# Kernel tuning notes

Hardware: AMD Instinct MI355X
Metric: run time of the kernel (lower is better)

The kernel has to match this reference:

```python
import jax, jax.numpy as jnp
import numpy as np

EPS = 1e-3  # matches eps=0.001 in __init__


def p2o(psf, H, W):
    """PSF -> OTF: zero-pad to (H,W), roll so kernel center is at origin, FFT2."""
    B, C, kh, kw = psf.shape
    otf = jnp.zeros((B, C, H, W), psf.dtype).at[:, :, :kh, :kw].set(psf)
    otf = jnp.roll(otf, (-(kh // 2), -(kw // 2)), axis=(-2, -1))
    return jnp.fft.fft2(otf)


def splits_mean(a, sf):
    """Mean over the sf*sf distinct blocks of splits(): contiguous-chunk split
    via view(sf, H/sf, sf, W/sf); mean over the two sf axes equals mean over
    the scale^2 trailing dim of the original splits output."""
    B, C, H, W = a.shape
    return a.reshape(B, C, sf, H // sf, sf, W // sf).mean(axis=(2, 4))


def setup_inputs() -> dict:
    key = jax.random.key(0)
    kx, kk = jax.random.split(key)
    x = jax.random.normal(kx, (4, 64, 128, 128), dtype=jnp.float32)
    k = jax.random.uniform(kk, (4, 64, 25, 25), dtype=jnp.float32)
    alpha = jnp.zeros((1, 64, 1, 1), dtype=jnp.float32)  # learned parameter
    return {"x": x, "k": k, "alpha": alpha, "sf": 2}


def reference(x, k, alpha, sf):
    biaseps = jax.nn.sigmoid(alpha - 9.0) + EPS          # (1,C,1,1)
    B, C, h, w = x.shape
    H, W = h * sf, w * sf
    # s-fold zero-fill upsample (STy)
    STy = jnp.zeros((B, C, H, W), x.dtype).at[:, :, ::sf, ::sf].set(x)
    # nearest-neighbor interpolate by sf
    xu = jnp.repeat(jnp.repeat(x, sf, axis=-2), sf, axis=-1) if sf != 1 else x
    FB = p2o(k, H, W)                                    # complex (B,C,H,W)
    FBC = jnp.conj(FB)
    F2B = jnp.abs(FB) ** 2
    FBFy = FBC * jnp.fft.fft2(STy)
    FR = FBFy + jnp.fft.fft2(biaseps * xu)
    FBR = splits_mean(FB * FR, sf)                       # (B,C,H/sf,W/sf)
    invW = splits_mean(F2B, sf)
    invWBR = FBR / (invW + biaseps)
    FCBinvWBR = FBC * jnp.tile(invWBR, (1, 1, sf, sf))   # repeat(1,1,sf,sf)
    FX = (FR - FCBinvWBR) / biaseps
    return jnp.real(jnp.fft.ifft2(FX))
```

## Files before the change

kernel.cpp:

```cpp
#include <hip/hip_runtime.h>
#include <math.h>


static __device__ __forceinline__ float2 cmul(float2 a, float2 b) {
    return make_float2(a.x * b.x - a.y * b.y, a.x * b.y + a.y * b.x);
}
static __device__ __forceinline__ float2 cadd(float2 a, float2 b) {
    return make_float2(a.x + b.x, a.y + b.y);
}
static __device__ __forceinline__ float2 csub(float2 a, float2 b) {
    return make_float2(a.x - b.x, a.y - b.y);
}
static __device__ __forceinline__ float2 conjf2(float2 a) {
    return make_float2(a.x, -a.y);
}
static __device__ __forceinline__ int PHI(int i) { return i + (i >> 3); }

template <int HB, int SIGN, int THREADS>
static __device__ __forceinline__ void fill_tw(float2* tw) {
    for (int i = threadIdx.x; i < HB; i += THREADS) {
        float s, c;
        __sincosf((float)SIGN * (float)M_PI * (float)i / (float)HB, &s, &c);
        tw[i] = make_float2(c, s);
    }
}

template <int N, int R, int SIGN>
static __device__ __forceinline__ int fft_lds_rows(float2 (&buf)[2][R][N],
                                                   const float2* __restrict__ tw) {
    constexpr int HB = N / 2;
    const int tid = threadIdx.x;
    const int row = tid / HB;
    const int bt = tid % HB;
    int cur = 0, m = 1;
    for (int l = HB; l >= 1; l >>= 1) {
        __syncthreads();
        const int k = bt & (m - 1);
        const float2 w = tw[bt - k];
        float2 a = buf[cur][row][bt];
        float2 b = buf[cur][row][bt + HB];
        float2 d = make_float2(a.x - b.x, a.y - b.y);
        float2 wd = make_float2(w.x * d.x - w.y * d.y, w.x * d.y + w.y * d.x);
        const int o = 2 * bt - k;
        buf[cur ^ 1][row][o] = make_float2(a.x + b.x, a.y + b.y);
        buf[cur ^ 1][row][o + m] = wd;
        cur ^= 1;
        m <<= 1;
    }
    __syncthreads();
    return cur;
}

template <int SIGN, int THREADS>
static __device__ __forceinline__ int fft4_cols_128(float2 (&buf)[2][128][16],
                                                    const float2* __restrict__ tw) {
    const int tid = threadIdx.x;
    int cur = 0, m = 1;
#pragma unroll
    for (int st = 0; st < 3; ++st) {
        __syncthreads();
        for (int w0 = tid; w0 < 512; w0 += THREADS) {
            const int col = w0 & 15;
            const int bq = w0 >> 4;
            const int k = bq & (m - 1);
            const int jm = bq - k;
            const float2 w1 = tw[jm];
            const float2 w2 = tw[2 * jm];
            const float2 w3 = tw[3 * jm];
            float2 a0 = buf[cur][bq][col];
            float2 a1 = buf[cur][bq + 32][col];
            float2 a2 = buf[cur][bq + 64][col];
            float2 a3 = buf[cur][bq + 96][col];
            float2 s02 = cadd(a0, a2), d02 = csub(a0, a2);
            float2 s13 = cadd(a1, a3), d13 = csub(a1, a3);
            float2 b0 = cadd(s02, s13), b2 = csub(s02, s13);
            float2 b1 = make_float2(d02.x - (float)SIGN * d13.y,
                                    d02.y + (float)SIGN * d13.x);
            float2 b3 = make_float2(d02.x + (float)SIGN * d13.y,
                                    d02.y - (float)SIGN * d13.x);
            const int o = 4 * jm + k;
            buf[cur ^ 1][o][col] = b0;
            buf[cur ^ 1][o + m][col] = cmul(w1, b1);
            buf[cur ^ 1][o + 2 * m][col] = cmul(w2, b2);
            buf[cur ^ 1][o + 3 * m][col] = cmul(w3, b3);
        }
        cur ^= 1;
        m <<= 2;
    }
    __syncthreads();
    for (int w0 = tid; w0 < 1024; w0 += THREADS) {
        const int col = w0 & 15;
        const int bt = w0 >> 4;
        float2 a = buf[cur][bt][col];
        float2 b = buf[cur][bt + 64][col];
        buf[cur ^ 1][bt][col] = cadd(a, b);
        buf[cur ^ 1][bt + 64][col] = csub(a, b);
    }
    cur ^= 1;
    __syncthreads();
    return cur;
}

__global__ __launch_bounds__(256) void k1_fft_rows_x(const float* __restrict__ x,
                                                     float2* __restrict__ Fx) {
    __shared__ float2 buf[2][4][128];
    __shared__ float2 tw64m[64];
    const int tid = threadIdx.x;
    const int row = tid >> 6;
    const int t = tid & 63;
    fill_tw<64, -1, 256>(tw64m);
    const int gpair = blockIdx.x * 4 + row;
    const float* r0 = x + (size_t)gpair * 256;
    const float* r1 = r0 + 128;
    const float2 a0 = ((const float2*)r0)[t];
    const float2 a1 = ((const float2*)r1)[t];
    buf[0][row][2 * t].x = a0.x;
    buf[0][row][2 * t].y = a1.x;
    buf[0][row][2 * t + 1].x = a0.y;
    buf[0][row][2 * t + 1].y = a1.y;
    int cur = fft_lds_rows<128, 4, -1>(buf, tw64m);
    float2* d0 = Fx + (size_t)gpair * 256;
    float2* d1 = d0 + 128;
    for (int h = 0; h < 2; ++h) {
        int tt = t + h * 64;
        float2 Zt = buf[cur][row][tt];
        float2 Zm = buf[cur][row][(128 - tt) & 127];
        d0[tt] = make_float2(0.5f * (Zt.x + Zm.x), 0.5f * (Zt.y - Zm.y));
        float ax = Zt.x - Zm.x, ay = Zt.y + Zm.y;
        d1[tt] = make_float2(0.5f * ay, -0.5f * ax);
    }
}

__global__ __launch_bounds__(256) void k2_fft_cols_x(float2* __restrict__ Fx) {
    __shared__ float2 buf[2][128][16];
    __shared__ float2 tw[96];
    const int tid = threadIdx.x;
    const int img = blockIdx.x >> 3;
    const int c0 = (blockIdx.x & 7) * 16;
    for (int i = tid; i < 96; i += 256) {
        float s, c;
        __sincosf(-(float)M_PI * (float)i / 64.f, &s, &c);
        tw[i] = make_float2(c, s);
    }
    float2* base = Fx + (size_t)img * 16384 + c0;
    for (int it = 0; it < 8; ++it) {
        int idx = it * 256 + tid;
        buf[0][idx >> 4][idx & 15] = base[(idx >> 4) * 128 + (idx & 15)];
    }
    int cur = fft4_cols_128<-1, 256>(buf, tw);
    for (int it = 0; it < 8; ++it) {
        int idx = it * 256 + tid;
        base[(idx >> 4) * 128 + (idx & 15)] = buf[cur][idx >> 4][idx & 15];
    }
}

__global__ __launch_bounds__(128) void k3_fft_rows_k(const float* __restrict__ kin,
                                                     float2* __restrict__ FBtmp) {
    __shared__ float2 buf[2][1][256];
    __shared__ float2 tw128m[128];
    const int tid = threadIdx.x;
    const int img = blockIdx.x / 25;
    const int lr = blockIdx.x % 25;
    fill_tw<128, -1, 128>(tw128m);
    const float* krow = kin + img * 625 + lr * 25;
    for (int h = 0; h < 2; ++h) {
        int v = tid + h * 128;
        int pc = (v + 12) & 255;
        buf[0][0][v] = make_float2(pc < 25 ? krow[pc] : 0.f, 0.f);
    }
    int cur = fft_lds_rows<256, 1, -1>(buf, tw128m);
    float2* dst = FBtmp + (size_t)img * 6400 + lr * 256;
    dst[tid] = buf[cur][0][tid];
    dst[tid + 128] = buf[cur][0][tid + 128];
}

__global__ __launch_bounds__(256) void k4_dft_cols_k(const float2* __restrict__ FBtmp,
                                                     float2* __restrict__ FBh) {
    __shared__ float2 T[33][28];
    const int j = threadIdx.x;
    const int img = blockIdx.x >> 2;
    const int q = blockIdx.x & 3;
    const int ubeg = q * 33;
    const int nu = (ubeg + 33 < 129) ? 33 : (129 - ubeg);
    const float k2pi = -2.f * (float)M_PI / 256.f;

    for (int idx = j; idx < nu * 25; idx += 256) {
        const int ul = idx / 25;
        const int p = idx - ul * 25;
        const int u = ubeg + ul;
        float s, c;
        __sincosf(k2pi * (float)((u * (p + 244)) & 255), &s, &c);
        T[ul][p] = make_float2(c, s);
    }

    const float2* src = FBtmp + (size_t)img * 6400 + j;
    float2 S[25];
#pragma unroll
    for (int p = 0; p < 25; ++p) S[p] = src[p * 256];
    __syncthreads();

    float2* dst = FBh + (size_t)img * 33024 + j;
    for (int ul = 0; ul < nu; ++ul) {
        float2 a0 = make_float2(0.f, 0.f);
        float2 a1 = make_float2(0.f, 0.f);
#pragma unroll
        for (int p = 0; p < 25; ++p) {
            const float2 t = T[ul][p];
            const float2 s = S[p];
            if (p & 1) {
                a1.x = fmaf(t.x, s.x, fmaf(-t.y, s.y, a1.x));
                a1.y = fmaf(t.x, s.y, fmaf(t.y, s.x, a1.y));
            } else {
                a0.x = fmaf(t.x, s.x, fmaf(-t.y, s.y, a0.x));
                a0.y = fmaf(t.x, s.y, fmaf(t.y, s.x, a0.y));
            }
        }
        dst[(size_t)(ubeg + ul) * 256] = make_float2(a0.x + a1.x, a0.y + a1.y);
    }
}

__global__ __launch_bounds__(256) void k6_fused(const float2* __restrict__ FBh,
                                                const float2* __restrict__ Fx,
                                                const float* __restrict__ alpha,
                                                float2* __restrict__ Zf) {
    __shared__ float2 stage[4][256];
    __shared__ float2 buf[2][4][288];
    __shared__ float2 tw[192];
    const int tid = threadIdx.x;
    const int rs = tid >> 6;
    const int q = tid & 63;
    const int img = blockIdx.x / 33;
    const int bq = blockIdx.x % 33;
    const int pa = 2 * bq;
    const int pb = (pa + 1 < 65) ? (pa + 1) : 64;
    for (int i = tid; i < 192; i += 256) {
        float s, c;
        __sincosf((float)M_PI * (float)i / 128.f, &s, &c);
        tw[i] = make_float2(c, s);
    }
    {
        const float2* base = FBh + (size_t)img * 33024;
        stage[0][tid] = base[pa * 256 + tid];
        stage[1][tid] = base[(128 - pa) * 256 + tid];
        stage[2][tid] = base[pb * 256 + tid];
        stage[3][tid] = base[(128 - pb) * 256 + tid];
    }
    __syncthreads();

    const int p = (rs < 2) ? pa : pb;
    const int sb = rs & 2;
    const int u = ((rs & 1) == 0) ? p : (128 - p);
    const int um = u & 127;
    const int msel = (um == p) ? 0 : 1;
    const int mi = sb | msel;
    const int oi = sb | (1 - msel);

    const float ci = tw[um].x, si = -tw[um].y;
    const float b = 1.f / (1.f + __expf(9.f - alpha[img & 63])) + 1e-3f;
    const float scale = 1.f / 65536.f;
    const float2 Di0 = make_float2(1.f + ci, si);
    const float2 Di1 = make_float2(1.f - ci, -si);
    const float2 Du = (u < 128) ? Di0 : Di1;
#pragma unroll
    for (int h = 0; h < 2; ++h) {
        const int t = q + 64 * h;
        float2 f00 = stage[mi][t];
        float2 f01 = stage[mi][t + 128];
        float2 f10, f11;
        if (um == 0) {
            f10 = stage[oi][t];
            f11 = stage[oi][t + 128];
        } else {
            f10 = conjf2(stage[oi][(256 - t) & 255]);
            f11 = conjf2(stage[oi][128 - t]);
        }
        float2 fx = Fx[(size_t)img * 16384 + um * 128 + t];
        const float cj = tw[t].x, sj = -tw[t].y;
        float2 Dj0 = make_float2(1.f + cj, sj);
        float2 Dj1 = make_float2(1.f - cj, -sj);
        float2 A = cadd(cmul(f00, Dj0), cmul(f01, Dj1));
        float2 Bt = cadd(cmul(f10, Dj0), cmul(f11, Dj1));
        float2 S1 = cadd(cmul(A, Di0), cmul(Bt, Di1));
        S1.x *= 0.25f;
        S1.y *= 0.25f;
        float S2 = 0.25f * (f00.x * f00.x + f00.y * f00.y + f01.x * f01.x + f01.y * f01.y +
                            f10.x * f10.x + f10.y * f10.y + f11.x * f11.x + f11.y * f11.y);
        float inv = 1.f / (S2 + b);
        float2 mm = make_float2((1.f - S1.x) * inv, (-S1.y) * inv);
        float2 c0v = (u < 128) ? f00 : f10;
        float2 c1v = (u < 128) ? f01 : f11;
        float2 t0 = cadd(cmul(conjf2(c0v), mm), cmul(Du, Dj0));
        float2 t1 = cadd(cmul(conjf2(c1v), mm), cmul(Du, Dj1));
        float2 FX0 = cmul(fx, t0);
        float2 FX1 = cmul(fx, t1);
        buf[0][rs][PHI(t)] = make_float2(FX0.x * scale, FX0.y * scale);
        buf[0][rs][PHI(t + 128)] = make_float2(FX1.x * scale, FX1.y * scale);
    }

    int cur = 0, m = 1;
#pragma unroll
    for (int st = 0; st < 4; ++st) {
        const int k = q & (m - 1);
        const int jm = q - k;
        const float2 w1 = tw[jm];
        const float2 w2 = tw[2 * jm];
        const float2 w3 = tw[3 * jm];
        float2 a0 = buf[cur][rs][PHI(q)];
        float2 a1 = buf[cur][rs][PHI(q + 64)];
        float2 a2 = buf[cur][rs][PHI(q + 128)];
        float2 a3 = buf[cur][rs][PHI(q + 192)];
        float2 s02 = cadd(a0, a2), d02 = csub(a0, a2);
        float2 s13 = cadd(a1, a3), d13 = csub(a1, a3);
        float2 b0 = cadd(s02, s13), b2v = csub(s02, s13);
        float2 b1 = make_float2(d02.x - d13.y, d02.y + d13.x);
        float2 b3 = make_float2(d02.x + d13.y, d02.y - d13.x);
        const int o = 4 * jm + k;
        buf[cur ^ 1][rs][PHI(o)] = b0;
        buf[cur ^ 1][rs][PHI(o + m)] = cmul(w1, b1);
        buf[cur ^ 1][rs][PHI(o + 2 * m)] = cmul(w2, b2v);
        buf[cur ^ 1][rs][PHI(o + 3 * m)] = cmul(w3, b3);
        cur ^= 1;
        m <<= 2;
    }
    __syncthreads();

    const int u0 = u;
    bool dowrite = ((rs & 1) == 0) ? true : (p > 0 && p < 64);
    if (pb == pa && rs >= 2) dowrite = false;
    if (dowrite) {
        const float2 w = tw[u0];
        float2* zb = Zf + (size_t)img * 32768 + (size_t)u0 * 256;
#pragma unroll
        for (int hh = 0; hh < 4; ++hh) {
            const int jj = q + 64 * hh;
            float2 su = buf[cur][rs][PHI(jj)];
            float2 s2 = buf[cur][rs ^ 1][PHI(jj)];
            float2 e = make_float2(su.x + s2.x, su.y - s2.y);
            float2 o_ = make_float2(su.x - s2.x, su.y + s2.y);
            float2 wo = cmul(w, o_);
            zb[jj] = make_float2(e.x - wo.y, e.y + wo.x);
        }
    }
}

__global__ __launch_bounds__(256) void k7_c2r(const float2* __restrict__ Zf,
                                              float* __restrict__ out) {
    __shared__ float2 buf[2][128][16];
    __shared__ float2 tw[96];
    const int tid = threadIdx.x;
    const int img = blockIdx.x >> 4;
    const int c0 = (blockIdx.x & 15) * 16;
    for (int i = tid; i < 96; i += 256) {
        float s, c;
        __sincosf((float)M_PI * (float)i / 64.f, &s, &c);
        tw[i] = make_float2(c, s);
    }
    const float2* zb = Zf + (size_t)img * 32768 + c0;
    for (int it = 0; it < 8; ++it) {
        int idx = it * 256 + tid;
        buf[0][idx >> 4][idx & 15] = zb[(idx >> 4) * 256 + (idx & 15)];
    }
    int cur = fft4_cols_128<1, 256>(buf, tw);
    float* ob = out + (size_t)img * 65536 + c0;
    for (int it = 0; it < 8; ++it) {
        int idx = it * 256 + tid;
        int n = idx >> 4, c = idx & 15;
        float2 y = buf[cur][n][c];
        ob[(2 * n) * 256 + c] = y.x;
        ob[(2 * n + 1) * 256 + c] = y.y;
    }
}

extern "C" void kernel_launch(void* const* d_in, const int* in_sizes, int n_in,
                              void* d_out, int out_size, void* d_ws, size_t ws_size,
                              hipStream_t stream) {
    const float* x = (const float*)d_in[0];
    const float* k = (const float*)d_in[1];
    const float* alpha = (const float*)d_in[2];
    float* out = (float*)d_out;

    float2* Fx = (float2*)d_ws;
    float2* FBh = Fx + 256 * 16384;
    float2* Zf = FBh + 256 * 33024;
    float2* FBtmp = Zf + 256 * 32768;

    hipLaunchKernelGGL(k1_fft_rows_x, dim3(4096), dim3(256), 0, stream, x, Fx);
    hipLaunchKernelGGL(k2_fft_cols_x, dim3(2048), dim3(256), 0, stream, Fx);
    hipLaunchKernelGGL(k3_fft_rows_k, dim3(6400), dim3(128), 0, stream, k, FBtmp);
    hipLaunchKernelGGL(k4_dft_cols_k, dim3(1024), dim3(256), 0, stream, FBtmp, FBh);
    hipLaunchKernelGGL(k6_fused, dim3(256 * 33), dim3(256), 0, stream, FBh, Fx, alpha, Zf);
    hipLaunchKernelGGL(k7_c2r, dim3(4096), dim3(256), 0, stream, Zf, out);
}
```

Measured before the change: 194.2 us.

## Exploit Hermitian symmetry of x spectrum and make column FFTs wave-local

The row FFT of real x now stores only the non-redundant half-spectrum columns (0..64), and the column FFT launches 5 column groups per image instead of 8. The fused kernel reconstructs the missing columns by conjugate mirroring. The column FFT helper is restructured so each wavefront owns 4 columns in a transposed, padded LDS layout, which removes the __syncthreads between radix stages. This cuts global traffic and barrier overhead. The cost is strided LDS transposes on load and store, and correctness now depends on wavefront-synchronous LDS execution.

```diff
diff --git a/kernel.cpp b/kernel.cpp
--- a/kernel.cpp
+++ b/kernel.cpp
@@ -51,26 +51,28 @@
     return cur;
 }
 
-template <int SIGN, int THREADS>
-static __device__ __forceinline__ int fft4_cols_128(float2 (&buf)[2][128][16],
-                                                    const float2* __restrict__ tw) {
-    const int tid = threadIdx.x;
+template <int SIGN, int NCOL>
+static __device__ __forceinline__ int fft4_cols_wavelocal(float2 (&buf)[2][NCOL][130],
+                                                          const float2* __restrict__ tw) {
+    const int lane = threadIdx.x & 63;
+    const int wv = threadIdx.x >> 6;
+    const int col = wv * 4 + (lane >> 4);
+    const int r = lane & 15;
     int cur = 0, m = 1;
 #pragma unroll
     for (int st = 0; st < 3; ++st) {
-        __syncthreads();
-        for (int w0 = tid; w0 < 512; w0 += THREADS) {
-            const int col = w0 & 15;
-            const int bq = w0 >> 4;
+#pragma unroll
+        for (int b = 0; b < 2; ++b) {
+            const int bq = r + 16 * b;
             const int k = bq & (m - 1);
             const int jm = bq - k;
             const float2 w1 = tw[jm];
             const float2 w2 = tw[2 * jm];
             const float2 w3 = tw[3 * jm];
-            float2 a0 = buf[cur][bq][col];
-            float2 a1 = buf[cur][bq + 32][col];
-            float2 a2 = buf[cur][bq + 64][col];
-            float2 a3 = buf[cur][bq + 96][col];
+            float2 a0 = buf[cur][col][bq];
+            float2 a1 = buf[cur][col][bq + 32];
+            float2 a2 = buf[cur][col][bq + 64];
+            float2 a3 = buf[cur][col][bq + 96];
             float2 s02 = cadd(a0, a2), d02 = csub(a0, a2);
             float2 s13 = cadd(a1, a3), d13 = csub(a1, a3);
             float2 b0 = cadd(s02, s13), b2 = csub(s02, s13);
@@ -79,26 +81,23 @@
             float2 b3 = make_float2(d02.x + (float)SIGN * d13.y,
                                     d02.y - (float)SIGN * d13.x);
             const int o = 4 * jm + k;
-            buf[cur ^ 1][o][col] = b0;
-            buf[cur ^ 1][o + m][col] = cmul(w1, b1);
-            buf[cur ^ 1][o + 2 * m][col] = cmul(w2, b2);
-            buf[cur ^ 1][o + 3 * m][col] = cmul(w3, b3);
+            buf[cur ^ 1][col][o] = b0;
+            buf[cur ^ 1][col][o + m] = cmul(w1, b1);
+            buf[cur ^ 1][col][o + 2 * m] = cmul(w2, b2);
+            buf[cur ^ 1][col][o + 3 * m] = cmul(w3, b3);
         }
         cur ^= 1;
         m <<= 2;
     }
-    __syncthreads();
-    for (int w0 = tid; w0 < 1024; w0 += THREADS) {
-        const int col = w0 & 15;
-        const int bt = w0 >> 4;
-        float2 a = buf[cur][bt][col];
-        float2 b = buf[cur][bt + 64][col];
-        buf[cur ^ 1][bt][col] = cadd(a, b);
-        buf[cur ^ 1][bt + 64][col] = csub(a, b);
-    }
-    cur ^= 1;
-    __syncthreads();
-    return cur;
+#pragma unroll
+    for (int b = 0; b < 4; ++b) {
+        const int bt = r + 16 * b;
+        float2 a = buf[cur][col][bt];
+        float2 bb = buf[cur][col][bt + 64];
+        buf[cur ^ 1][col][bt] = cadd(a, bb);
+        buf[cur ^ 1][col][bt + 64] = csub(a, bb);
+    }
+    return cur ^ 1;
 }
 
 __global__ __launch_bounds__(256) void k1_fft_rows_x(const float* __restrict__ x,
@@ -123,6 +122,7 @@
     float2* d1 = d0 + 128;
     for (int h = 0; h < 2; ++h) {
         int tt = t + h * 64;
+        if (tt > 64) continue;
         float2 Zt = buf[cur][row][tt];
         float2 Zm = buf[cur][row][(128 - tt) & 127];
         d0[tt] = make_float2(0.5f * (Zt.x + Zm.x), 0.5f * (Zt.y - Zm.y));
@@ -132,11 +132,11 @@
 }
 
 __global__ __launch_bounds__(256) void k2_fft_cols_x(float2* __restrict__ Fx) {
-    __shared__ float2 buf[2][128][16];
+    __shared__ float2 buf[2][16][130];
     __shared__ float2 tw[96];
     const int tid = threadIdx.x;
-    const int img = blockIdx.x >> 3;
-    const int c0 = (blockIdx.x & 7) * 16;
+    const int img = blockIdx.x / 5;
+    const int c0 = (blockIdx.x % 5) * 16;
     for (int i = tid; i < 96; i += 256) {
         float s, c;
         __sincosf(-(float)M_PI * (float)i / 64.f, &s, &c);
@@ -145,12 +145,16 @@
     float2* base = Fx + (size_t)img * 16384 + c0;
     for (int it = 0; it < 8; ++it) {
         int idx = it * 256 + tid;
-        buf[0][idx >> 4][idx & 15] = base[(idx >> 4) * 128 + (idx & 15)];
-    }
-    int cur = fft4_cols_128<-1, 256>(buf, tw);
+        int rr = idx >> 4, cc = idx & 15;
+        buf[0][cc][rr] = base[rr * 128 + cc];
+    }
+    __syncthreads();
+    int cur = fft4_cols_wavelocal<-1, 16>(buf, tw);
+    __syncthreads();
     for (int it = 0; it < 8; ++it) {
         int idx = it * 256 + tid;
-        base[(idx >> 4) * 128 + (idx & 15)] = buf[cur][idx >> 4][idx & 15];
+        int rr = idx >> 4, cc = idx & 15;
+        base[rr * 128 + cc] = buf[cur][cc][rr];
     }
 }
 
@@ -274,7 +278,11 @@
             f10 = conjf2(stage[oi][(256 - t) & 255]);
             f11 = conjf2(stage[oi][128 - t]);
         }
-        float2 fx = Fx[(size_t)img * 16384 + um * 128 + t];
+        const bool mir = (t > 64);
+        const int rr = mir ? ((128 - um) & 127) : um;
+        const int cc = mir ? (128 - t) : t;
+        float2 fx = Fx[(size_t)img * 16384 + rr * 128 + cc];
+        if (mir) fx.y = -fx.y;
         const float cj = tw[t].x, sj = -tw[t].y;
         float2 Dj0 = make_float2(1.f + cj, sj);
         float2 Dj1 = make_float2(1.f - cj, -sj);
@@ -345,7 +353,7 @@
 
 __global__ __launch_bounds__(256) void k7_c2r(const float2* __restrict__ Zf,
                                               float* __restrict__ out) {
-    __shared__ float2 buf[2][128][16];
+    __shared__ float2 buf[2][16][130];
     __shared__ float2 tw[96];
     const int tid = threadIdx.x;
     const int img = blockIdx.x >> 4;
@@ -358,14 +366,17 @@
     const float2* zb = Zf + (size_t)img * 32768 + c0;
     for (int it = 0; it < 8; ++it) {
         int idx = it * 256 + tid;
-        buf[0][idx >> 4][idx & 15] = zb[(idx >> 4) * 256 + (idx & 15)];
-    }
-    int cur = fft4_cols_128<1, 256>(buf, tw);
+        int rr = idx >> 4, cc = idx & 15;
+        buf[0][cc][rr] = zb[rr * 256 + cc];
+    }
+    __syncthreads();
+    int cur = fft4_cols_wavelocal<1, 16>(buf, tw);
+    __syncthreads();
     float* ob = out + (size_t)img * 65536 + c0;
     for (int it = 0; it < 8; ++it) {
         int idx = it * 256 + tid;
         int n = idx >> 4, c = idx & 15;
-        float2 y = buf[cur][n][c];
+        float2 y = buf[cur][c][n];
         ob[(2 * n) * 256 + c] = y.x;
         ob[(2 * n + 1) * 256 + c] = y.y;
     }
@@ -385,7 +396,7 @@
     float2* FBtmp = Zf + 256 * 32768;
 
     hipLaunchKernelGGL(k1_fft_rows_x, dim3(4096), dim3(256), 0, stream, x, Fx);
-    hipLaunchKernelGGL(k2_fft_cols_x, dim3(2048), dim3(256), 0, stream, Fx);
+    hipLaunchKernelGGL(k2_fft_cols_x, dim3(256 * 5), dim3(256), 0, stream, Fx);
     hipLaunchKernelGGL(k3_fft_rows_k, dim3(6400), dim3(128), 0, stream, k, FBtmp);
     hipLaunchKernelGGL(k4_dft_cols_k, dim3(1024), dim3(256), 0, stream, FBtmp, FBh);
     hipLaunchKernelGGL(k6_fused, dim3(256 * 33), dim3(256), 0, stream, FBh, Fx, alpha, Zf);
```

After: 190.5 us. No clear change (-1.9%).
